# Performance work log

Measured on AMD Instinct MI355X. Metric: run time of the kernel, lower is better.

The kernel has to match this reference:

```python
import jax, jax.numpy as jnp
import numpy as np

B, H, L, D = 2, 8, 2048, 64

def setup_inputs() -> dict:
    key = jax.random.key(0)
    kq, kk, kv = jax.random.split(key, 3)
    q = jax.random.normal(kq, (B, H, L, D), dtype=jnp.float32)
    k = jax.random.normal(kk, (B, H, L, D), dtype=jnp.float32)
    v = jax.random.normal(kv, (B, H, L, D), dtype=jnp.float32)
    return {"q": q, "k": k, "v": v}

def reference(q, k, v):
    # attn = q @ k^T  -> [B, H, Lq, Lk]  (no softmax, no scaling, as in source)
    attn = jnp.einsum('bhqd,bhkd->bhqk', q, k)
    # output = attn @ v -> [B, H, Lq, D]
    out = jnp.einsum('bhqk,bhkd->bhqd', attn, v)
    return out
```

## Files before the change

### kernel.cpp

```cpp
#include <hip/hip_runtime.h>
#include <hip/hip_bf16.h>

#define BHN    16
#define LSEQ   2048
#define DDIM   64
#define CHUNK  64
#define NCHUNK (LSEQ / CHUNK)
#define NPART  (BHN * NCHUNK)

typedef unsigned short ushort8 __attribute__((ext_vector_type(8)));
typedef __bf16        bf16x8  __attribute__((ext_vector_type(8)));
typedef float         f32x4   __attribute__((ext_vector_type(4)));

__device__ __forceinline__ unsigned short f2bf(float f) {
    unsigned int u = __float_as_uint(f);
    u = u + 0x7FFFu + ((u >> 16) & 1u);
    return (unsigned short)(u >> 16);
}

union Frag { ushort8 u; bf16x8 b; };

__global__ __launch_bounds__(256, 2) void k1_ktv(const float* __restrict__ Km,
                                                 const float* __restrict__ Vm,
                                                 float* __restrict__ P) {
    __shared__ float R[16384];

    const int pid   = blockIdx.x;
    const int bh    = pid >> 5;
    const int chunk = pid & 31;
    const int t     = threadIdx.x;
    const int w     = t >> 6;
    const int lane  = t & 63;
    const int a     = lane & 7;
    const int b     = lane >> 3;

    const float* Kbase = Km + (size_t)bh * LSEQ * DDIM + (size_t)chunk * CHUNK * DDIM;
    const float* Vbase = Vm + (size_t)bh * LSEQ * DDIM + (size_t)chunk * CHUNK * DDIM;

    float acc[8][8];
    #pragma unroll
    for (int i = 0; i < 8; ++i)
        #pragma unroll
        for (int j = 0; j < 8; ++j) acc[i][j] = 0.f;

    const float* Kw = Kbase + (w * 16) * DDIM;
    const float* Vw = Vbase + (w * 16) * DDIM;

    #pragma unroll 4
    for (int l = 0; l < 16; ++l) {
        float4 k0 = *(const float4*)(Kw + l * DDIM + a * 8);
        float4 k1 = *(const float4*)(Kw + l * DDIM + a * 8 + 4);
        float4 v0 = *(const float4*)(Vw + l * DDIM + b * 8);
        float4 v1 = *(const float4*)(Vw + l * DDIM + b * 8 + 4);
        float kk[8] = {k0.x, k0.y, k0.z, k0.w, k1.x, k1.y, k1.z, k1.w};
        float vv[8] = {v0.x, v0.y, v0.z, v0.w, v1.x, v1.y, v1.z, v1.w};
        #pragma unroll
        for (int j2 = 0; j2 < 8; ++j2)
            #pragma unroll
            for (int j1 = 0; j1 < 8; ++j1)
                acc[j2][j1] = fmaf(kk[j1], vv[j2], acc[j2][j1]);
    }

    #pragma unroll
    for (int j2 = 0; j2 < 8; ++j2) {
        int row = b * 8 + j2;
        int pc  = (a ^ j2) * 8;
        float* dst = R + w * 4096 + row * 64 + pc;
        *(float4*)(dst)     = float4{acc[j2][0], acc[j2][1], acc[j2][2], acc[j2][3]};
        *(float4*)(dst + 4) = float4{acc[j2][4], acc[j2][5], acc[j2][6], acc[j2][7]};
    }
    __syncthreads();

    float* Pout = P + (size_t)pid * 4096;
    #pragma unroll
    for (int i = 0; i < 16; ++i) {
        int e   = t + i * 256;
        int row = e >> 6;
        int col = e & 63;
        int pcc = col ^ ((row & 7) << 3);
        int idx = row * 64 + pcc;
        Pout[e] = R[idx] + R[4096 + idx] + R[8192 + idx] + R[12288 + idx];
    }
}

__global__ __launch_bounds__(256) void k2_reduce(const float* __restrict__ P,
                                                 unsigned short* __restrict__ MT) {
    const int blk = blockIdx.x;
    const int bh  = blk >> 4;
    const int seg = blk & 15;
    const int e   = seg * 256 + threadIdx.x;
    const float* Pb = P + (size_t)bh * 32 * 4096 + e;
    float s = 0.f;
    #pragma unroll
    for (int c = 0; c < 32; ++c)
        s += Pb[(size_t)c * 4096];
    MT[(size_t)bh * 4096 + e] = f2bf(s);
}

__global__ __launch_bounds__(256) void k3_qm(const float* __restrict__ Q,
                                             const unsigned short* __restrict__ MT,
                                             float* __restrict__ Out) {
    const int pid  = blockIdx.x;
    const int bh   = pid >> 5;
    const int rb   = pid & 31;
    const int t    = threadIdx.x;
    const int w    = t >> 6;
    const int lane = t & 63;
    const int q0   = rb * 64 + w * 16;
    const int r    = lane & 15;
    const int g    = lane >> 4;

    const float* Qb = Q + (size_t)bh * LSEQ * DDIM;

    Frag afrag[2];
    #pragma unroll
    for (int s = 0; s < 2; ++s) {
        const float* qp = Qb + (size_t)(q0 + r) * DDIM + s * 32 + g * 8;
        float4 x0 = *(const float4*)qp;
        float4 x1 = *(const float4*)(qp + 4);
        afrag[s].u = (ushort8){f2bf(x0.x), f2bf(x0.y), f2bf(x0.z), f2bf(x0.w),
                               f2bf(x1.x), f2bf(x1.y), f2bf(x1.z), f2bf(x1.w)};
    }

    const unsigned short* Mb = MT + (size_t)bh * 4096;
    f32x4 acc[4];
    #pragma unroll
    for (int nt = 0; nt < 4; ++nt) {
        acc[nt] = (f32x4){0.f, 0.f, 0.f, 0.f};
        #pragma unroll
        for (int s = 0; s < 2; ++s) {
            Frag bfrag;
            bfrag.u = *(const ushort8*)(Mb + (nt * 16 + r) * 64 + s * 32 + g * 8);
            acc[nt] = __builtin_amdgcn_mfma_f32_16x16x32_bf16(afrag[s].b, bfrag.b,
                                                              acc[nt], 0, 0, 0);
        }
    }

    float* Ob = Out + (size_t)bh * LSEQ * DDIM;
    #pragma unroll
    for (int nt = 0; nt < 4; ++nt)
        #pragma unroll
        for (int j = 0; j < 4; ++j)
            Ob[(size_t)(q0 + g * 4 + j) * DDIM + nt * 16 + r] = acc[nt][j];
}

extern "C" void kernel_launch(void* const* d_in, const int* in_sizes, int n_in,
                              void* d_out, int out_size, void* d_ws, size_t ws_size,
                              hipStream_t stream) {
    const float* q = (const float*)d_in[0];
    const float* k = (const float*)d_in[1];
    const float* v = (const float*)d_in[2];
    float* out = (float*)d_out;

    float*          P  = (float*)d_ws;
    unsigned short* MT = (unsigned short*)((char*)d_ws +
                          (size_t)NPART * 4096 * sizeof(float));

    k1_ktv   <<<NPART,    256, 0, stream>>>(k, v, P);
    k2_reduce<<<256,      256, 0, stream>>>(P, MT);
    k3_qm    <<<BHN * 32, 256, 0, stream>>>(q, MT, out);
}
```

Measured before the change: 85.74 us.

## Fuse partial reduction into QM kernel and double K^T V chunk size

```diff
diff --git a/kernel.cpp b/kernel.cpp
--- a/kernel.cpp
+++ b/kernel.cpp
@@ -4,7 +4,7 @@
 #define BHN    16
 #define LSEQ   2048
 #define DDIM   64
-#define CHUNK  64
+#define CHUNK  128
 #define NCHUNK (LSEQ / CHUNK)
 #define NPART  (BHN * NCHUNK)
 
@@ -20,14 +20,14 @@
 
 union Frag { ushort8 u; bf16x8 b; };
 
-__global__ __launch_bounds__(256, 2) void k1_ktv(const float* __restrict__ Km,
-                                                 const float* __restrict__ Vm,
-                                                 float* __restrict__ P) {
+__global__ __launch_bounds__(256) void k1_ktv(const float* __restrict__ Km,
+                                              const float* __restrict__ Vm,
+                                              float* __restrict__ P) {
     __shared__ float R[16384];
 
     const int pid   = blockIdx.x;
-    const int bh    = pid >> 5;
-    const int chunk = pid & 31;
+    const int bh    = pid >> 4;
+    const int chunk = pid & 15;
     const int t     = threadIdx.x;
     const int w     = t >> 6;
     const int lane  = t & 63;
@@ -43,11 +43,11 @@
         #pragma unroll
         for (int j = 0; j < 8; ++j) acc[i][j] = 0.f;
 
-    const float* Kw = Kbase + (w * 16) * DDIM;
-    const float* Vw = Vbase + (w * 16) * DDIM;
+    const float* Kw = Kbase + (w * 32) * DDIM;
+    const float* Vw = Vbase + (w * 32) * DDIM;
 
     #pragma unroll 4
-    for (int l = 0; l < 16; ++l) {
+    for (int l = 0; l < 32; ++l) {
         float4 k0 = *(const float4*)(Kw + l * DDIM + a * 8);
         float4 k1 = *(const float4*)(Kw + l * DDIM + a * 8 + 4);
         float4 v0 = *(const float4*)(Vw + l * DDIM + b * 8);
@@ -83,65 +83,71 @@
     }
 }
 
-__global__ __launch_bounds__(256) void k2_reduce(const float* __restrict__ P,
-                                                 unsigned short* __restrict__ MT) {
-    const int blk = blockIdx.x;
-    const int bh  = blk >> 4;
-    const int seg = blk & 15;
-    const int e   = seg * 256 + threadIdx.x;
-    const float* Pb = P + (size_t)bh * 32 * 4096 + e;
-    float s = 0.f;
-    #pragma unroll
-    for (int c = 0; c < 32; ++c)
-        s += Pb[(size_t)c * 4096];
-    MT[(size_t)bh * 4096 + e] = f2bf(s);
-}
+__global__ __launch_bounds__(512) void k3_qm(const float* __restrict__ Q,
+                                             const float* __restrict__ P,
+                                             float* __restrict__ Out) {
+    __shared__ unsigned short MTs[4096];
 
-__global__ __launch_bounds__(256) void k3_qm(const float* __restrict__ Q,
-                                             const unsigned short* __restrict__ MT,
-                                             float* __restrict__ Out) {
-    const int pid  = blockIdx.x;
-    const int bh   = pid >> 5;
-    const int rb   = pid & 31;
-    const int t    = threadIdx.x;
-    const int w    = t >> 6;
-    const int lane = t & 63;
-    const int q0   = rb * 64 + w * 16;
-    const int r    = lane & 15;
-    const int g    = lane >> 4;
+    const int bid = blockIdx.x;
+    const int bh  = bid >> 4;
+    const int qb  = bid & 15;
+    const int t   = threadIdx.x;
 
-    const float* Qb = Q + (size_t)bh * LSEQ * DDIM;
+    {
+        const float* Pb = P + (size_t)bh * 16 * 4096;
+        f32x4 s0 = (f32x4){0.f, 0.f, 0.f, 0.f};
+        f32x4 s1 = (f32x4){0.f, 0.f, 0.f, 0.f};
+        #pragma unroll 4
+        for (int c = 0; c < 16; ++c) {
+            const f32x4* p4 = (const f32x4*)(Pb + (size_t)c * 4096) + t * 2;
+            s0 += p4[0];
+            s1 += p4[1];
+        }
+        const int row = t >> 3;
+        const int cg  = t & 7;
+        ushort8 u = (ushort8){f2bf(s0[0]), f2bf(s0[1]), f2bf(s0[2]), f2bf(s0[3]),
+                              f2bf(s1[0]), f2bf(s1[1]), f2bf(s1[2]), f2bf(s1[3])};
+        *(ushort8*)(MTs + row * 64 + ((cg ^ (row & 7)) << 3)) = u;
+    }
+    __syncthreads();
 
-    Frag afrag[2];
-    #pragma unroll
-    for (int s = 0; s < 2; ++s) {
-        const float* qp = Qb + (size_t)(q0 + r) * DDIM + s * 32 + g * 8;
-        float4 x0 = *(const float4*)qp;
-        float4 x1 = *(const float4*)(qp + 4);
-        afrag[s].u = (ushort8){f2bf(x0.x), f2bf(x0.y), f2bf(x0.z), f2bf(x0.w),
-                               f2bf(x1.x), f2bf(x1.y), f2bf(x1.z), f2bf(x1.w)};
-    }
+    {
+        const int w    = t >> 6;
+        const int lane = t & 63;
+        const int r    = lane & 15;
+        const int g    = lane >> 4;
+        const int q0   = qb * 128 + w * 16;
 
-    const unsigned short* Mb = MT + (size_t)bh * 4096;
-    f32x4 acc[4];
-    #pragma unroll
-    for (int nt = 0; nt < 4; ++nt) {
-        acc[nt] = (f32x4){0.f, 0.f, 0.f, 0.f};
+        const float* Qb = Q + (size_t)bh * LSEQ * DDIM;
+
+        Frag afrag[2];
         #pragma unroll
         for (int s = 0; s < 2; ++s) {
-            Frag bfrag;
-            bfrag.u = *(const ushort8*)(Mb + (nt * 16 + r) * 64 + s * 32 + g * 8);
-            acc[nt] = __builtin_amdgcn_mfma_f32_16x16x32_bf16(afrag[s].b, bfrag.b,
-                                                              acc[nt], 0, 0, 0);
+            const float* qp = Qb + (size_t)(q0 + r) * DDIM + s * 32 + g * 8;
+            float4 x0 = *(const float4*)qp;
+            float4 x1 = *(const float4*)(qp + 4);
+            afrag[s].u = (ushort8){f2bf(x0.x), f2bf(x0.y), f2bf(x0.z), f2bf(x0.w),
+                                   f2bf(x1.x), f2bf(x1.y), f2bf(x1.z), f2bf(x1.w)};
+        }
+
+        float* Ob = Out + (size_t)bh * LSEQ * DDIM;
+        #pragma unroll
+        for (int nt = 0; nt < 4; ++nt) {
+            f32x4 acc = (f32x4){0.f, 0.f, 0.f, 0.f};
+            #pragma unroll
+            for (int s = 0; s < 2; ++s) {
+                const int brow = nt * 16 + r;
+                const int bg   = (s * 4 + g) ^ (r & 7);
+                Frag bfrag;
+                bfrag.u = *(const ushort8*)(MTs + brow * 64 + bg * 8);
+                acc = __builtin_amdgcn_mfma_f32_16x16x32_bf16(afrag[s].b, bfrag.b,
+                                                              acc, 0, 0, 0);
+            }
+            #pragma unroll
+            for (int j = 0; j < 4; ++j)
+                Ob[(size_t)(q0 + g * 4 + j) * DDIM + nt * 16 + r] = acc[j];
         }
     }
-
-    float* Ob = Out + (size_t)bh * LSEQ * DDIM;
-    #pragma unroll
-    for (int nt = 0; nt < 4; ++nt)
-        #pragma unroll
-        for (int j = 0; j < 4; ++j)
-            Ob[(size_t)(q0 + g * 4 + j) * DDIM + nt * 16 + r] = acc[nt][j];
 }
 
 extern "C" void kernel_launch(void* const* d_in, const int* in_sizes, int n_in,
@@ -152,11 +158,8 @@
     const float* v = (const float*)d_in[2];
     float* out = (float*)d_out;
 
-    float*          P  = (float*)d_ws;
-    unsigned short* MT = (unsigned short*)((char*)d_ws +
-                          (size_t)NPART * 4096 * sizeof(float));
+    float* P = (float*)d_ws;
 
-    k1_ktv   <<<NPART,    256, 0, stream>>>(k, v, P);
-    k2_reduce<<<256,      256, 0, stream>>>(P, MT);
-    k3_qm    <<<BHN * 32, 256, 0, stream>>>(q, MT, out);
+    k1_ktv<<<NPART, 256, 0, stream>>>(k, v, P);
+    k3_qm <<<NPART, 512, 0, stream>>>(q, P, out);
 }
```

New measurement: 85.31 us. Within noise of the previous version (-0.5%).
